# Kernel optimization log

Hardware: AMD Instinct MI355X
Metric: run time of the kernel (lower is better)

## Reference

```python
import jax, jax.numpy as jnp
import numpy as np

MOMENTUM = 0.1
C_DIM = 5


def setup_inputs() -> dict:
    key = jax.random.key(0)
    k1, k2, k3 = jax.random.split(key, 3)
    B, C, H, W = 16, 256, 128, 128
    im = jax.random.normal(k1, (B, C, H, W), dtype=jnp.float32)
    running_mean = jnp.zeros((2 * C_DIM, C), dtype=jnp.float32)
    running_std = jnp.ones((2 * C_DIM, C), dtype=jnp.float32)
    c_trg = jax.random.randint(k2, (B, C_DIM), 0, 2, dtype=jnp.int32)
    c_org = jax.random.randint(k3, (B, C_DIM), 0, 2, dtype=jnp.int32)
    return {"im": im, "running_mean": running_mean, "running_std": running_std,
            "c_trg": c_trg, "c_org": c_org}


def reference(im, running_mean, running_std, c_trg, c_org):
    B, C, H, W = im.shape
    N = H * W
    # per-sample per-channel instance stats; torch.std_mean uses correction=1
    mean = jnp.mean(im, axis=(2, 3))                      # [B, C]
    var = jnp.sum((im - mean[:, :, None, None]) ** 2, axis=(2, 3)) / (N - 1)
    std = jnp.sqrt(var)                                   # [B, C]

    ct = c_trg.astype(bool)
    co = c_org.astype(bool)
    c_trg_full = jnp.concatenate([ct, ~ct], axis=1)       # [B, 2*c_dim]
    c_org_full = jnp.concatenate([co, ~co], axis=1)       # [B, 2*c_dim]

    m = jnp.float32(MOMENTUM)

    # sequential EMA update of running buffers, in batch order (matches torch loop)
    def step(carry, xs):
        rm, rs = carry
        std_n, mean_n, org_n = xs                         # [C], [C], [2*c_dim]
        msk = org_n[:, None]                              # [2*c_dim, 1]
        rs = jnp.where(msk, rs * (1 - m) + std_n[None, :] * m, rs)
        rm = jnp.where(msk, rm * (1 - m) + mean_n[None, :] * m, rm)
        return (rm, rs), None

    (rm_final, rs_final), _ = jax.lax.scan(
        step, (running_mean, running_std), (std, mean, c_org_full))

    # per-sample gather: mean of selected buffer rows. Exactly c_dim rows are
    # selected per sample (each attribute contributes itself or its negation).
    sel = c_trg_full.astype(im.dtype)                     # [B, 2*c_dim]
    cnt = jnp.sum(sel, axis=1, keepdims=True)             # [B, 1] (== c_dim)
    trg_std = (sel @ rs_final) / cnt                      # [B, C]
    trg_mean = (sel @ rm_final) / cnt                     # [B, C]

    def bc(x):  # [B, C] -> [B, C, 1, 1]
        return x[:, :, None, None]

    return (im - bc(mean)) / bc(std) * bc(trg_std) + bc(trg_mean)
```

## Files before the change

### kernel.cpp

```cpp
#include <hip/hip_runtime.h>
#include <math.h>

#define CDIM 5
constexpr int B_ = 16;
constexpr int C_ = 256;
constexpr int HW_ = 128 * 128;
constexpr float MOM = 0.1f;

using f32x4 = __attribute__((ext_vector_type(4))) float;

__global__ __launch_bounds__(256) void cin_stats(const float* __restrict__ im,
                                                 float* __restrict__ ws_mean,
                                                 float* __restrict__ ws_std) {
    const int plane = blockIdx.x;
    const f32x4* p4 = (const f32x4*)(im + (size_t)plane * HW_);
    const int t = threadIdx.x;

    float sum = 0.f, sumsq = 0.f;
    #pragma unroll
    for (int it = 0; it < 16; ++it) {
        f32x4 v = p4[it * 256 + t];
        sum   += v.x + v.y + v.z + v.w;
        sumsq += v.x * v.x + v.y * v.y + v.z * v.z + v.w * v.w;
    }

    #pragma unroll
    for (int off = 32; off > 0; off >>= 1) {
        sum   += __shfl_down(sum, off, 64);
        sumsq += __shfl_down(sumsq, off, 64);
    }

    __shared__ float s_sum[4], s_sq[4];
    const int wave = t >> 6;
    if ((t & 63) == 0) { s_sum[wave] = sum; s_sq[wave] = sumsq; }
    __syncthreads();

    if (t == 0) {
        float s = s_sum[0] + s_sum[1] + s_sum[2] + s_sum[3];
        float q = s_sq[0] + s_sq[1] + s_sq[2] + s_sq[3];
        float mean = s / (float)HW_;
        float var = fmaxf(q - s * mean, 0.f) / (float)(HW_ - 1);
        ws_mean[plane] = mean;
        ws_std[plane]  = sqrtf(var);
    }
}

__global__ __launch_bounds__(256) void cin_scan(const float* __restrict__ running_mean,
                                                const float* __restrict__ running_std,
                                                const int* __restrict__ c_trg,
                                                const int* __restrict__ c_org,
                                                const float* __restrict__ ws_mean,
                                                const float* __restrict__ ws_std,
                                                float* __restrict__ ws_scale,
                                                float* __restrict__ ws_shift) {
    const int t = threadIdx.x;

    float rm[2 * CDIM], rs[2 * CDIM];
    #pragma unroll
    for (int r = 0; r < 2 * CDIM; ++r) {
        rm[r] = running_mean[r * C_ + t];
        rs[r] = running_std [r * C_ + t];
    }

    for (int n = 0; n < B_; ++n) {
        const float mn = ws_mean[n * C_ + t];
        const float sd = ws_std [n * C_ + t];
        #pragma unroll
        for (int r = 0; r < 2 * CDIM; ++r) {
            const int k = (r < CDIM) ? r : r - CDIM;
            const int bit = c_org[n * CDIM + k];
            const bool msk = (r < CDIM) ? (bit != 0) : (bit == 0);
            if (msk) {
                rs[r] = rs[r] * (1.f - MOM) + sd * MOM;
                rm[r] = rm[r] * (1.f - MOM) + mn * MOM;
            }
        }
    }

    __shared__ float s_rm[2 * CDIM * C_], s_rs[2 * CDIM * C_];
    #pragma unroll
    for (int r = 0; r < 2 * CDIM; ++r) {
        s_rm[r * C_ + t] = rm[r];
        s_rs[r * C_ + t] = rs[r];
    }
    __syncthreads();

    for (int b = 0; b < B_; ++b) {
        float cnt = 0.f, tm = 0.f, ts = 0.f;
        #pragma unroll
        for (int r = 0; r < 2 * CDIM; ++r) {
            const int k = (r < CDIM) ? r : r - CDIM;
            const int bit = c_trg[b * CDIM + k];
            const bool sel = (r < CDIM) ? (bit != 0) : (bit == 0);
            if (sel) {
                cnt += 1.f;
                tm  += s_rm[r * C_ + t];
                ts  += s_rs[r * C_ + t];
            }
        }
        tm /= cnt;
        ts /= cnt;
        const int plane = b * C_ + t;
        const float mean = ws_mean[plane];
        const float std  = ws_std [plane];
        const float scale = ts / std;
        ws_scale[plane] = scale;
        ws_shift[plane] = tm - mean * scale;
    }
}

__global__ __launch_bounds__(256) void cin_norm(const float* __restrict__ im,
                                                const float* __restrict__ ws_scale,
                                                const float* __restrict__ ws_shift,
                                                float* __restrict__ out) {
    const int plane = blockIdx.x;
    const float scale = ws_scale[plane];
    const float shift = ws_shift[plane];
    const f32x4* p4 = (const f32x4*)(im + (size_t)plane * HW_);
    f32x4*       o4 = (f32x4*)(out + (size_t)plane * HW_);
    const int t = threadIdx.x;

    #pragma unroll
    for (int it = 0; it < 16; ++it) {
        f32x4 v = p4[it * 256 + t];
        f32x4 r;
        r.x = fmaf(v.x, scale, shift);
        r.y = fmaf(v.y, scale, shift);
        r.z = fmaf(v.z, scale, shift);
        r.w = fmaf(v.w, scale, shift);
        __builtin_nontemporal_store(r, &o4[it * 256 + t]);
    }
}

extern "C" void kernel_launch(void* const* d_in, const int* in_sizes, int n_in,
                              void* d_out, int out_size, void* d_ws, size_t ws_size,
                              hipStream_t stream) {
    const float* im           = (const float*)d_in[0];
    const float* running_mean = (const float*)d_in[1];
    const float* running_std  = (const float*)d_in[2];
    const int*   c_trg        = (const int*)d_in[3];
    const int*   c_org        = (const int*)d_in[4];
    float* out = (float*)d_out;

    float* ws       = (float*)d_ws;
    float* ws_mean  = ws;
    float* ws_std   = ws + B_ * C_;
    float* ws_scale = ws + 2 * B_ * C_;
    float* ws_shift = ws + 3 * B_ * C_;

    const int planes = B_ * C_;

    cin_stats<<<planes, 256, 0, stream>>>(im, ws_mean, ws_std);
    cin_scan<<<1, 256, 0, stream>>>(running_mean, running_std, c_trg, c_org,
                                    ws_mean, ws_std, ws_scale, ws_shift);
    cin_norm<<<planes, 256, 0, stream>>>(im, ws_scale, ws_shift, out);
}
```

Baseline: 135.4 us.

## Parallelize scan over buffer rows and fuse target gather into norm kernel

The EMA scan kernel now runs one block per running-buffer row instead of one block in total, which shortens its serial critical path. The per-sample target mean/std gather and the scale/shift computation move into each block of the norm kernel. The norm kernel also walks planes in reverse order, so the planes cin_stats touched last, which are more likely still in cache, are read first. The cost is a small amount of redundant gather work in each norm block.

```diff
diff --git a/kernel.cpp b/kernel.cpp
--- a/kernel.cpp
+++ b/kernel.cpp
@@ -47,75 +47,60 @@
 
 __global__ __launch_bounds__(256) void cin_scan(const float* __restrict__ running_mean,
                                                 const float* __restrict__ running_std,
-                                                const int* __restrict__ c_trg,
                                                 const int* __restrict__ c_org,
                                                 const float* __restrict__ ws_mean,
                                                 const float* __restrict__ ws_std,
-                                                float* __restrict__ ws_scale,
-                                                float* __restrict__ ws_shift) {
-    const int t = threadIdx.x;
+                                                float* __restrict__ ws_rm,
+                                                float* __restrict__ ws_rs) {
+    const int r = blockIdx.x;
+    const int c = threadIdx.x;
 
-    float rm[2 * CDIM], rs[2 * CDIM];
-    #pragma unroll
-    for (int r = 0; r < 2 * CDIM; ++r) {
-        rm[r] = running_mean[r * C_ + t];
-        rs[r] = running_std [r * C_ + t];
-    }
+    float rm = running_mean[r * C_ + c];
+    float rs = running_std [r * C_ + c];
+    const int k = (r < CDIM) ? r : r - CDIM;
 
     for (int n = 0; n < B_; ++n) {
-        const float mn = ws_mean[n * C_ + t];
-        const float sd = ws_std [n * C_ + t];
-        #pragma unroll
-        for (int r = 0; r < 2 * CDIM; ++r) {
-            const int k = (r < CDIM) ? r : r - CDIM;
-            const int bit = c_org[n * CDIM + k];
-            const bool msk = (r < CDIM) ? (bit != 0) : (bit == 0);
-            if (msk) {
-                rs[r] = rs[r] * (1.f - MOM) + sd * MOM;
-                rm[r] = rm[r] * (1.f - MOM) + mn * MOM;
-            }
+        const int bit = c_org[n * CDIM + k];
+        const bool msk = (r < CDIM) ? (bit != 0) : (bit == 0);
+        if (msk) {
+            rs = rs * (1.f - MOM) + ws_std [n * C_ + c] * MOM;
+            rm = rm * (1.f - MOM) + ws_mean[n * C_ + c] * MOM;
         }
     }
-
-    __shared__ float s_rm[2 * CDIM * C_], s_rs[2 * CDIM * C_];
-    #pragma unroll
-    for (int r = 0; r < 2 * CDIM; ++r) {
-        s_rm[r * C_ + t] = rm[r];
-        s_rs[r * C_ + t] = rs[r];
-    }
-    __syncthreads();
-
-    for (int b = 0; b < B_; ++b) {
-        float cnt = 0.f, tm = 0.f, ts = 0.f;
-        #pragma unroll
-        for (int r = 0; r < 2 * CDIM; ++r) {
-            const int k = (r < CDIM) ? r : r - CDIM;
-            const int bit = c_trg[b * CDIM + k];
-            const bool sel = (r < CDIM) ? (bit != 0) : (bit == 0);
-            if (sel) {
-                cnt += 1.f;
-                tm  += s_rm[r * C_ + t];
-                ts  += s_rs[r * C_ + t];
-            }
-        }
-        tm /= cnt;
-        ts /= cnt;
-        const int plane = b * C_ + t;
-        const float mean = ws_mean[plane];
-        const float std  = ws_std [plane];
-        const float scale = ts / std;
-        ws_scale[plane] = scale;
-        ws_shift[plane] = tm - mean * scale;
-    }
+    ws_rm[r * C_ + c] = rm;
+    ws_rs[r * C_ + c] = rs;
 }
 
 __global__ __launch_bounds__(256) void cin_norm(const float* __restrict__ im,
-                                                const float* __restrict__ ws_scale,
-                                                const float* __restrict__ ws_shift,
+                                                const float* __restrict__ ws_mean,
+                                                const float* __restrict__ ws_std,
+                                                const float* __restrict__ ws_rm,
+                                                const float* __restrict__ ws_rs,
+                                                const int* __restrict__ c_trg,
                                                 float* __restrict__ out) {
-    const int plane = blockIdx.x;
-    const float scale = ws_scale[plane];
-    const float shift = ws_shift[plane];
+    const int plane = (B_ * C_ - 1) - blockIdx.x;
+    const int b = plane >> 8;
+    const int c = plane & (C_ - 1);
+
+    float tm = 0.f, ts = 0.f, cnt = 0.f;
+    #pragma unroll
+    for (int r = 0; r < 2 * CDIM; ++r) {
+        const int k = (r < CDIM) ? r : r - CDIM;
+        const int bit = c_trg[b * CDIM + k];
+        const bool sel = (r < CDIM) ? (bit != 0) : (bit == 0);
+        if (sel) {
+            cnt += 1.f;
+            tm  += ws_rm[r * C_ + c];
+            ts  += ws_rs[r * C_ + c];
+        }
+    }
+    tm /= cnt;
+    ts /= cnt;
+    const float mean  = ws_mean[plane];
+    const float std   = ws_std [plane];
+    const float scale = ts / std;
+    const float shift = tm - mean * scale;
+
     const f32x4* p4 = (const f32x4*)(im + (size_t)plane * HW_);
     f32x4*       o4 = (f32x4*)(out + (size_t)plane * HW_);
     const int t = threadIdx.x;
@@ -142,16 +127,17 @@
     const int*   c_org        = (const int*)d_in[4];
     float* out = (float*)d_out;
 
-    float* ws       = (float*)d_ws;
-    float* ws_mean  = ws;
-    float* ws_std   = ws + B_ * C_;
-    float* ws_scale = ws + 2 * B_ * C_;
-    float* ws_shift = ws + 3 * B_ * C_;
+    float* ws      = (float*)d_ws;
+    float* ws_mean = ws;
+    float* ws_std  = ws + B_ * C_;
+    float* ws_rm   = ws + 2 * B_ * C_;
+    float* ws_rs   = ws + 2 * B_ * C_ + 2 * CDIM * C_;
 
     const int planes = B_ * C_;
 
     cin_stats<<<planes, 256, 0, stream>>>(im, ws_mean, ws_std);
-    cin_scan<<<1, 256, 0, stream>>>(running_mean, running_std, c_trg, c_org,
-                                    ws_mean, ws_std, ws_scale, ws_shift);
-    cin_norm<<<planes, 256, 0, stream>>>(im, ws_scale, ws_shift, out);
+    cin_scan<<<2 * CDIM, 256, 0, stream>>>(running_mean, running_std, c_org,
+                                           ws_mean, ws_std, ws_rm, ws_rs);
+    cin_norm<<<planes, 256, 0, stream>>>(im, ws_mean, ws_std, ws_rm, ws_rs,
+                                         c_trg, out);
 }
```

New measurement: 128.3 us. 5.2% less time.
